# Optimization experiments

Measured on AMD Instinct MI355X. Metric: run time of the kernel, lower is better.

The kernel has to match this reference:

```python
import jax, jax.numpy as jnp
import numpy as np

FEATURE_MAPS = 128
POOLING_OUT = 4
KERNAL_LEN = 3
EMB_DIM = 300
CLASSES = 7
B, L, N = 64, 512, 2048


def setup_inputs() -> dict:
    key = jax.random.key(0)
    ks = jax.random.split(key, 10)
    sentence = jax.random.normal(ks[0], (B, 1, L, EMB_DIM), dtype=jnp.float32)
    # ROIs: [x1, x2) spans within [0, L], span length in [1, 32]
    x1 = jax.random.randint(ks[1], (N,), 0, L - 33)
    span = jax.random.randint(ks[2], (N,), 1, 33)
    rois = jnp.stack([x1, x1 + span], axis=1).astype(jnp.int64)
    ridx = jax.random.randint(ks[3], (N,), 0, B).astype(jnp.int64)
    s = 0.02
    conv_w = jax.random.normal(ks[4], (FEATURE_MAPS, 1, KERNAL_LEN, EMB_DIM), dtype=jnp.float32) * s
    conv_b = jax.random.normal(ks[5], (FEATURE_MAPS,), dtype=jnp.float32) * s
    FF = FEATURE_MAPS * POOLING_OUT
    fc1_w = jax.random.normal(ks[6], (FF, FF), dtype=jnp.float32) * s
    fc1_b = jax.random.normal(ks[7], (FF,), dtype=jnp.float32) * s
    cls_w = jax.random.normal(ks[8], (CLASSES + 1, FF), dtype=jnp.float32) * s
    cls_b = jax.random.normal(ks[9], (CLASSES + 1,), dtype=jnp.float32) * s
    return {"sentence": sentence, "rois": rois, "ridx": ridx,
            "conv_w": conv_w, "conv_b": conv_b, "fc1_w": fc1_w, "fc1_b": fc1_b,
            "cls_w": cls_w, "cls_b": cls_b}


def reference(sentence, rois, ridx, conv_w, conv_b, fc1_w, fc1_b, cls_w, cls_b):
    # conv1: Conv2d(1->F, (K, D), padding=(1,0)) + ReLU -> [B, F, L, 1]
    feat = jax.lax.conv_general_dilated(
        sentence, conv_w, window_strides=(1, 1),
        padding=((1, 1), (0, 0)),
        dimension_numbers=("NCHW", "OIHW", "NCHW"))
    feat = jax.nn.relu(feat + conv_b[None, :, None, None])[..., 0]  # [B, F, L]
    # ROI max-pool over each span [x1, x2) of the length dim (vectorized)
    g = feat[ridx]                                  # [N, F, L]
    pos = jnp.arange(feat.shape[-1])
    mask = (pos[None, :] >= rois[:, 0:1]) & (pos[None, :] < rois[:, 1:2])  # [N, L]
    neg = jnp.finfo(feat.dtype).min
    pooled = jnp.max(jnp.where(mask[:, None, :], g, neg), axis=-1)  # [N, F]
    # AdaptiveMaxPool2d((1, P)) with input width 1 replicates each channel P times,
    # and .view flattening is channel-major -> jnp.repeat along last axis matches.
    x = jnp.repeat(pooled, POOLING_OUT, axis=-1)    # [N, F*P]
    x = x @ fc1_w.T + fc1_b
    return x @ cls_w.T + cls_b                      # [N, CLASSES+1]
```

## Files before the change

### kernel.cpp

```cpp
#include <hip/hip_runtime.h>
#include <hip/hip_bf16.h>

#define FMAPS 128
#define SEQL  512
#define BATCH 64
#define EMB   300
#define NKC   30
#define NROI  2048
#define FFDIM 512
#define NCLS  8

#define MF_BLOCKS   32
#define B2_BLOCKS   1
#define WPAD_BLOCKS 480

typedef short bf16x8 __attribute__((ext_vector_type(8)));
typedef float f32x4  __attribute__((ext_vector_type(4)));

static __device__ __forceinline__ float relu_(float x) { return x > 0.f ? x : 0.f; }
static __device__ __forceinline__ uint bf16bits(float f) {
    __hip_bfloat16 h = __float2bfloat16(f);
    return (uint)*reinterpret_cast<ushort*>(&h);
}

__global__ __launch_bounds__(256) void prep(
    const float* __restrict__ conv_w, const float* __restrict__ cls_w,
    const float* __restrict__ fc1_w, const float* __restrict__ fc1_b,
    const float* __restrict__ cls_b,
    ushort* __restrict__ wf, float* __restrict__ Mfp, float* __restrict__ b2) {
    __shared__ float red[2][128];
    const int tid = threadIdx.x;
    int blk = blockIdx.x;

    if (blk < MF_BLOCKS) {
        const int c = blk & 7, q = blk >> 3;
        const int g = tid & 127, ih = tid >> 7;
        const int i0 = q * 128 + ih * 64;
        float s = 0.f;
        for (int i = i0; i < i0 + 64; ++i) {
            float4 w4 = *(const float4*)(fc1_w + (size_t)i * FFDIM + 4 * g);
            s = fmaf(cls_w[c * FFDIM + i], (w4.x + w4.y) + (w4.z + w4.w), s);
        }
        red[ih][g] = s;
        __syncthreads();
        if (tid < 128) Mfp[(q * 8 + c) * FMAPS + tid] = red[0][tid] + red[1][tid];
        return;
    }
    blk -= MF_BLOCKS;

    if (blk < B2_BLOCKS) {
        const int c = tid >> 5, l32 = tid & 31;
        float s = 0.f;
        for (int i = l32; i < FFDIM; i += 32)
            s = fmaf(cls_w[c * FFDIM + i], fc1_b[i], s);
#pragma unroll
        for (int off = 16; off; off >>= 1) s += __shfl_xor(s, off, 64);
        if (l32 == 0) b2[c] = s + cls_b[c];
        return;
    }
    blk -= B2_BLOCKS;

    {
        int idx = blk * 256 + tid;
        int j    = idx & 7;
        int lane = (idx >> 3) & 63;
        int nt   = (idx >> 9) & 7;
        int kc   = idx >> 12;
        int f = nt * 16 + (lane & 15);
        int k = kc * 32 + (lane >> 4) * 8 + j;
        int kr = k / 320, d = k % 320;
        float v = (d < EMB) ? conv_w[f * 900 + kr * 300 + d] : 0.f;
        wf[idx] = (ushort)bf16bits(v);
    }
}

__global__ __launch_bounds__(256) void conv_mfma(
    const float* __restrict__ sent, const ushort* __restrict__ wf,
    const float* __restrict__ cb, float* __restrict__ feat) {
    __shared__ __align__(16) ushort XL[66 * 320];
    const int t    = threadIdx.x;
    const int lane = t & 63;
    const int wn   = t >> 6;
    const int b    = blockIdx.x >> 3;
    const int l0   = (blockIdx.x & 7) << 6;
    const int mrow = lane & 15;
    const int koct = lane >> 4;

#pragma unroll
    for (int it = 0; it < 11; ++it) {
        int c = it * 256 + t;
        if (c < 2640) {
            int j = c / 40, i16 = c - j * 40;
            int sr = l0 + j - 1;
            int d0 = i16 * 8;
            float4 va = make_float4(0.f, 0.f, 0.f, 0.f), vb = va;
            if ((unsigned)sr < (unsigned)SEQL) {
                const float* srow = sent + ((size_t)b * SEQL + sr) * EMB;
                if (d0 < EMB)     va = *(const float4*)(srow + d0);
                if (d0 + 4 < EMB) vb = *(const float4*)(srow + d0 + 4);
            }
            uint4 pk;
            pk.x = bf16bits(va.x) | (bf16bits(va.y) << 16);
            pk.y = bf16bits(va.z) | (bf16bits(va.w) << 16);
            pk.z = bf16bits(vb.x) | (bf16bits(vb.y) << 16);
            pk.w = bf16bits(vb.z) | (bf16bits(vb.w) << 16);
            *(uint4*)((char*)XL + j * 640 + ((i16 ^ (j & 7)) << 4)) = pk;
        }
    }
    __syncthreads();

    f32x4 acc[4][2] = {};
    const ushort* wlane = wf + (size_t)(wn * 2) * 512 + (size_t)lane * 8;

#pragma unroll
    for (int kr = 0; kr < 3; ++kr) {
        const int sj = (mrow + kr) & 7;
#pragma unroll
        for (int dc = 0; dc < 10; ++dc) {
            const int kc = kr * 10 + dc;
            bf16x8 a[4];
#pragma unroll
            for (int mr = 0; mr < 4; ++mr) {
                const int j = mr * 16 + mrow + kr;
                a[mr] = *(const bf16x8*)((const char*)XL + j * 640 +
                                         (((dc * 4 + koct) ^ sj) << 4));
            }
            const ushort* wk = wlane + (size_t)kc * 4096;
            bf16x8 b0 = *(const bf16x8*)(wk);
            bf16x8 b1 = *(const bf16x8*)(wk + 512);
#pragma unroll
            for (int mr = 0; mr < 4; ++mr) {
                acc[mr][0] = __builtin_amdgcn_mfma_f32_16x16x32_bf16(a[mr], b0, acc[mr][0], 0, 0, 0);
                acc[mr][1] = __builtin_amdgcn_mfma_f32_16x16x32_bf16(a[mr], b1, acc[mr][1], 0, 0, 0);
            }
        }
    }

#pragma unroll
    for (int nr = 0; nr < 2; ++nr) {
        const int f = wn * 32 + nr * 16 + mrow;
        const float bias = cb[f];
#pragma unroll
        for (int mr = 0; mr < 4; ++mr) {
            const int lb = l0 + mr * 16 + koct * 4;
#pragma unroll
            for (int r = 0; r < 4; ++r)
                feat[((size_t)b * SEQL + (lb + r)) * FMAPS + f] = relu_(acc[mr][nr][r] + bias);
        }
    }
}

__global__ __launch_bounds__(256) void roi_fc(
    const float* __restrict__ feat, const int* __restrict__ rois,
    const int* __restrict__ ridx, const float* __restrict__ Mfp,
    const float* __restrict__ b2, float* __restrict__ out) {
    const int w    = threadIdx.x >> 6;
    const int lane = threadIdx.x & 63;
    const int n    = blockIdx.x * 4 + w;
    const int x1 = rois[n * 2 + 0];
    const int x2 = rois[n * 2 + 1];
    const int bi = ridx[n];
    const int half = lane >> 5, c4 = lane & 31;

    const float* base = feat + (size_t)bi * SEQL * FMAPS + c4 * 4;
    float4 m = make_float4(-1e30f, -1e30f, -1e30f, -1e30f);
    for (int l = x1 + half; l < x2; l += 2) {
        float4 v = *(const float4*)(base + (size_t)l * FMAPS);
        m.x = fmaxf(m.x, v.x); m.y = fmaxf(m.y, v.y);
        m.z = fmaxf(m.z, v.z); m.w = fmaxf(m.w, v.w);
    }
    m.x = fmaxf(m.x, __shfl_xor(m.x, 32, 64));
    m.y = fmaxf(m.y, __shfl_xor(m.y, 32, 64));
    m.z = fmaxf(m.z, __shfl_xor(m.z, 32, 64));
    m.w = fmaxf(m.w, __shfl_xor(m.w, 32, 64));

    const float4* M4 = (const float4*)Mfp;
#pragma unroll
    for (int c = 0; c < 8; ++c) {
        float4 w0 = M4[(c) * 32 + c4];
        float4 w1 = M4[(8 + c) * 32 + c4];
        float4 w2 = M4[(16 + c) * 32 + c4];
        float4 w3 = M4[(24 + c) * 32 + c4];
        float4 wv;
        wv.x = (w0.x + w1.x) + (w2.x + w3.x);
        wv.y = (w0.y + w1.y) + (w2.y + w3.y);
        wv.z = (w0.z + w1.z) + (w2.z + w3.z);
        wv.w = (w0.w + w1.w) + (w2.w + w3.w);
        float p = m.x * wv.x + m.y * wv.y + m.z * wv.z + m.w * wv.w;
#pragma unroll
        for (int off = 16; off; off >>= 1) p += __shfl_xor(p, off, 64);
        if (lane == 0) out[n * NCLS + c] = p + b2[c];
    }
}

extern "C" void kernel_launch(void* const* d_in, const int* in_sizes, int n_in,
                              void* d_out, int out_size, void* d_ws, size_t ws_size,
                              hipStream_t stream) {
    const float* sentence = (const float*)d_in[0];
    const int*   rois     = (const int*)d_in[1];
    const int*   ridx     = (const int*)d_in[2];
    const float* conv_w   = (const float*)d_in[3];
    const float* conv_b   = (const float*)d_in[4];
    const float* fc1_w    = (const float*)d_in[5];
    const float* fc1_b    = (const float*)d_in[6];
    const float* cls_w    = (const float*)d_in[7];
    const float* cls_b    = (const float*)d_in[8];
    float* out = (float*)d_out;

    char* ws = (char*)d_ws;
    float*  Ft  = (float*)ws;
    ushort* Wf  = (ushort*)(ws + 16777216);
    float*  Mfp = (float*)(ws + 16777216 + 245760);
    float*  b2  = Mfp + 4096;

    hipLaunchKernelGGL(prep, dim3(MF_BLOCKS + B2_BLOCKS + WPAD_BLOCKS), dim3(256), 0, stream,
                       conv_w, cls_w, fc1_w, fc1_b, cls_b, Wf, Mfp, b2);
    hipLaunchKernelGGL(conv_mfma, dim3((BATCH * SEQL) / 64), dim3(256), 0, stream,
                       sentence, Wf, conv_b, Ft);
    hipLaunchKernelGGL(roi_fc, dim3(NROI / 4), dim3(256), 0, stream,
                       Ft, rois, ridx, Mfp, b2, out);
}
```

Measured before the change: 132.2 us.

## Fuse prep, conv and ROI/FC kernels into one persistent kernel with grid barriers

Merges the three launches (weight prep, MFMA convolution, ROI pool plus FC) into a single 512-block kernel separated by software grid barriers built on atomics. The goal is to remove per-launch overhead and inter-kernel gaps. The Mfp partial-sum computation is now split across 64 blocks instead of 32, and the ROI stage sums 8 partials. The barrier assumes all 512 blocks are co-resident, which launch_bounds(256,2) is meant to ensure; if they are not, it risks deadlock. It also adds a memset and the spin-wait cost.

```diff
diff --git a/kernel.cpp b/kernel.cpp
--- a/kernel.cpp
+++ b/kernel.cpp
@@ -5,14 +5,10 @@
 #define SEQL  512
 #define BATCH 64
 #define EMB   300
-#define NKC   30
 #define NROI  2048
 #define FFDIM 512
 #define NCLS  8
-
-#define MF_BLOCKS   32
-#define B2_BLOCKS   1
-#define WPAD_BLOCKS 480
+#define GRID  512
 
 typedef short bf16x8 __attribute__((ext_vector_type(8)));
 typedef float f32x4  __attribute__((ext_vector_type(4)));
@@ -23,45 +19,39 @@
     return (uint)*reinterpret_cast<ushort*>(&h);
 }
 
-__global__ __launch_bounds__(256) void prep(
-    const float* __restrict__ conv_w, const float* __restrict__ cls_w,
+static __device__ __forceinline__ void grid_barrier(uint* bar, int tid) {
+    __syncthreads();
+    if (tid == 0) {
+        __threadfence();
+        uint g = __hip_atomic_load(bar + 1, __ATOMIC_RELAXED, __HIP_MEMORY_SCOPE_AGENT);
+        uint a = __hip_atomic_fetch_add(bar, 1u, __ATOMIC_ACQ_REL, __HIP_MEMORY_SCOPE_AGENT);
+        if (a == GRID - 1) {
+            __hip_atomic_store(bar, 0u, __ATOMIC_RELAXED, __HIP_MEMORY_SCOPE_AGENT);
+            __hip_atomic_store(bar + 1, g + 1u, __ATOMIC_RELEASE, __HIP_MEMORY_SCOPE_AGENT);
+        } else {
+            while (__hip_atomic_load(bar + 1, __ATOMIC_ACQUIRE, __HIP_MEMORY_SCOPE_AGENT) == g) {
+                __builtin_amdgcn_s_sleep(8);
+            }
+        }
+        __threadfence();
+    }
+    __syncthreads();
+}
+
+__global__ __launch_bounds__(256, 2) void rcnn_fused(
+    const float* __restrict__ sent, const int* __restrict__ rois,
+    const int* __restrict__ ridx, const float* __restrict__ conv_w,
+    const float* __restrict__ cb, const float* __restrict__ cls_w,
     const float* __restrict__ fc1_w, const float* __restrict__ fc1_b,
     const float* __restrict__ cls_b,
-    ushort* __restrict__ wf, float* __restrict__ Mfp, float* __restrict__ b2) {
-    __shared__ float red[2][128];
-    const int tid = threadIdx.x;
-    int blk = blockIdx.x;
-
-    if (blk < MF_BLOCKS) {
-        const int c = blk & 7, q = blk >> 3;
-        const int g = tid & 127, ih = tid >> 7;
-        const int i0 = q * 128 + ih * 64;
-        float s = 0.f;
-        for (int i = i0; i < i0 + 64; ++i) {
-            float4 w4 = *(const float4*)(fc1_w + (size_t)i * FFDIM + 4 * g);
-            s = fmaf(cls_w[c * FFDIM + i], (w4.x + w4.y) + (w4.z + w4.w), s);
-        }
-        red[ih][g] = s;
-        __syncthreads();
-        if (tid < 128) Mfp[(q * 8 + c) * FMAPS + tid] = red[0][tid] + red[1][tid];
-        return;
-    }
-    blk -= MF_BLOCKS;
-
-    if (blk < B2_BLOCKS) {
-        const int c = tid >> 5, l32 = tid & 31;
-        float s = 0.f;
-        for (int i = l32; i < FFDIM; i += 32)
-            s = fmaf(cls_w[c * FFDIM + i], fc1_b[i], s);
-#pragma unroll
-        for (int off = 16; off; off >>= 1) s += __shfl_xor(s, off, 64);
-        if (l32 == 0) b2[c] = s + cls_b[c];
-        return;
-    }
-    blk -= B2_BLOCKS;
-
-    {
-        int idx = blk * 256 + tid;
+    ushort* __restrict__ wf, float* __restrict__ Mfp, float* __restrict__ b2,
+    float* __restrict__ feat, float* __restrict__ out, uint* __restrict__ bar) {
+    __shared__ __align__(16) ushort XL[66 * 320];
+    const int t   = threadIdx.x;
+    const int blk = blockIdx.x;
+
+    if (t < 240) {
+        int idx  = blk * 240 + t;
         int j    = idx & 7;
         int lane = (idx >> 3) & 63;
         int nt   = (idx >> 9) & 7;
@@ -72,124 +62,138 @@
         float v = (d < EMB) ? conv_w[f * 900 + kr * 300 + d] : 0.f;
         wf[idx] = (ushort)bf16bits(v);
     }
-}
-
-__global__ __launch_bounds__(256) void conv_mfma(
-    const float* __restrict__ sent, const ushort* __restrict__ wf,
-    const float* __restrict__ cb, float* __restrict__ feat) {
-    __shared__ __align__(16) ushort XL[66 * 320];
-    const int t    = threadIdx.x;
-    const int lane = t & 63;
-    const int wn   = t >> 6;
-    const int b    = blockIdx.x >> 3;
-    const int l0   = (blockIdx.x & 7) << 6;
-    const int mrow = lane & 15;
-    const int koct = lane >> 4;
-
-#pragma unroll
-    for (int it = 0; it < 11; ++it) {
-        int c = it * 256 + t;
-        if (c < 2640) {
-            int j = c / 40, i16 = c - j * 40;
-            int sr = l0 + j - 1;
-            int d0 = i16 * 8;
-            float4 va = make_float4(0.f, 0.f, 0.f, 0.f), vb = va;
-            if ((unsigned)sr < (unsigned)SEQL) {
-                const float* srow = sent + ((size_t)b * SEQL + sr) * EMB;
-                if (d0 < EMB)     va = *(const float4*)(srow + d0);
-                if (d0 + 4 < EMB) vb = *(const float4*)(srow + d0 + 4);
-            }
-            uint4 pk;
-            pk.x = bf16bits(va.x) | (bf16bits(va.y) << 16);
-            pk.y = bf16bits(va.z) | (bf16bits(va.w) << 16);
-            pk.z = bf16bits(vb.x) | (bf16bits(vb.y) << 16);
-            pk.w = bf16bits(vb.z) | (bf16bits(vb.w) << 16);
-            *(uint4*)((char*)XL + j * 640 + ((i16 ^ (j & 7)) << 4)) = pk;
-        }
-    }
-    __syncthreads();
-
-    f32x4 acc[4][2] = {};
-    const ushort* wlane = wf + (size_t)(wn * 2) * 512 + (size_t)lane * 8;
-
-#pragma unroll
-    for (int kr = 0; kr < 3; ++kr) {
-        const int sj = (mrow + kr) & 7;
-#pragma unroll
-        for (int dc = 0; dc < 10; ++dc) {
-            const int kc = kr * 10 + dc;
-            bf16x8 a[4];
+    if (blk < 64) {
+        float* red = (float*)XL;
+        const int c = blk & 7, q8 = blk >> 3;
+        const int g = t & 127, ih = t >> 7;
+        const int i0 = q8 * 64 + ih * 32;
+        float s = 0.f;
+        for (int i = i0; i < i0 + 32; ++i) {
+            float4 w4 = *(const float4*)(fc1_w + (size_t)i * FFDIM + 4 * g);
+            s = fmaf(cls_w[c * FFDIM + i], (w4.x + w4.y) + (w4.z + w4.w), s);
+        }
+        red[ih * 128 + g] = s;
+        __syncthreads();
+        if (t < 128) Mfp[(q8 * 8 + c) * FMAPS + t] = red[t] + red[128 + t];
+    } else if (blk == 64) {
+        const int c = t >> 5, l32 = t & 31;
+        float s = 0.f;
+        for (int i = l32; i < FFDIM; i += 32)
+            s = fmaf(cls_w[c * FFDIM + i], fc1_b[i], s);
+#pragma unroll
+        for (int off = 16; off; off >>= 1) s += __shfl_xor(s, off, 64);
+        if (l32 == 0) b2[c] = s + cls_b[c];
+    }
+    grid_barrier(bar, t);
+
+    {
+        const int lane = t & 63;
+        const int wn   = t >> 6;
+        const int b    = blk >> 3;
+        const int l0   = (blk & 7) << 6;
+        const int mrow = lane & 15;
+        const int koct = lane >> 4;
+
+#pragma unroll
+        for (int it = 0; it < 11; ++it) {
+            int c = it * 256 + t;
+            if (c < 2640) {
+                int j = c / 40, i16 = c - j * 40;
+                int sr = l0 + j - 1;
+                int d0 = i16 * 8;
+                float4 va = make_float4(0.f, 0.f, 0.f, 0.f), vb = va;
+                if ((unsigned)sr < (unsigned)SEQL) {
+                    const float* srow = sent + ((size_t)b * SEQL + sr) * EMB;
+                    if (d0 < EMB)     va = *(const float4*)(srow + d0);
+                    if (d0 + 4 < EMB) vb = *(const float4*)(srow + d0 + 4);
+                }
+                uint4 pk;
+                pk.x = bf16bits(va.x) | (bf16bits(va.y) << 16);
+                pk.y = bf16bits(va.z) | (bf16bits(va.w) << 16);
+                pk.z = bf16bits(vb.x) | (bf16bits(vb.y) << 16);
+                pk.w = bf16bits(vb.z) | (bf16bits(vb.w) << 16);
+                *(uint4*)((char*)XL + j * 640 + ((i16 ^ (j & 7)) << 4)) = pk;
+            }
+        }
+        __syncthreads();
+
+        f32x4 acc[4][2] = {};
+        const ushort* wlane = wf + (size_t)(wn * 2) * 512 + (size_t)lane * 8;
+
+#pragma unroll
+        for (int kr = 0; kr < 3; ++kr) {
+            const int sj = (mrow + kr) & 7;
+#pragma unroll
+            for (int dc = 0; dc < 10; ++dc) {
+                const int kc = kr * 10 + dc;
+                bf16x8 a[4];
+#pragma unroll
+                for (int mr = 0; mr < 4; ++mr) {
+                    const int j = mr * 16 + mrow + kr;
+                    a[mr] = *(const bf16x8*)((const char*)XL + j * 640 +
+                                             (((dc * 4 + koct) ^ sj) << 4));
+                }
+                const ushort* wk = wlane + (size_t)kc * 4096;
+                bf16x8 b0 = *(const bf16x8*)(wk);
+                bf16x8 b1 = *(const bf16x8*)(wk + 512);
+#pragma unroll
+                for (int mr = 0; mr < 4; ++mr) {
+                    acc[mr][0] = __builtin_amdgcn_mfma_f32_16x16x32_bf16(a[mr], b0, acc[mr][0], 0, 0, 0);
+                    acc[mr][1] = __builtin_amdgcn_mfma_f32_16x16x32_bf16(a[mr], b1, acc[mr][1], 0, 0, 0);
+                }
+            }
+        }
+
+#pragma unroll
+        for (int nr = 0; nr < 2; ++nr) {
+            const int f = wn * 32 + nr * 16 + mrow;
+            const float bias = cb[f];
 #pragma unroll
             for (int mr = 0; mr < 4; ++mr) {
-                const int j = mr * 16 + mrow + kr;
-                a[mr] = *(const bf16x8*)((const char*)XL + j * 640 +
-                                         (((dc * 4 + koct) ^ sj) << 4));
-            }
-            const ushort* wk = wlane + (size_t)kc * 4096;
-            bf16x8 b0 = *(const bf16x8*)(wk);
-            bf16x8 b1 = *(const bf16x8*)(wk + 512);
-#pragma unroll
-            for (int mr = 0; mr < 4; ++mr) {
-                acc[mr][0] = __builtin_amdgcn_mfma_f32_16x16x32_bf16(a[mr], b0, acc[mr][0], 0, 0, 0);
-                acc[mr][1] = __builtin_amdgcn_mfma_f32_16x16x32_bf16(a[mr], b1, acc[mr][1], 0, 0, 0);
-            }
-        }
-    }
-
-#pragma unroll
-    for (int nr = 0; nr < 2; ++nr) {
-        const int f = wn * 32 + nr * 16 + mrow;
-        const float bias = cb[f];
-#pragma unroll
-        for (int mr = 0; mr < 4; ++mr) {
-            const int lb = l0 + mr * 16 + koct * 4;
-#pragma unroll
-            for (int r = 0; r < 4; ++r)
-                feat[((size_t)b * SEQL + (lb + r)) * FMAPS + f] = relu_(acc[mr][nr][r] + bias);
-        }
-    }
-}
-
-__global__ __launch_bounds__(256) void roi_fc(
-    const float* __restrict__ feat, const int* __restrict__ rois,
-    const int* __restrict__ ridx, const float* __restrict__ Mfp,
-    const float* __restrict__ b2, float* __restrict__ out) {
-    const int w    = threadIdx.x >> 6;
-    const int lane = threadIdx.x & 63;
-    const int n    = blockIdx.x * 4 + w;
-    const int x1 = rois[n * 2 + 0];
-    const int x2 = rois[n * 2 + 1];
-    const int bi = ridx[n];
-    const int half = lane >> 5, c4 = lane & 31;
-
-    const float* base = feat + (size_t)bi * SEQL * FMAPS + c4 * 4;
-    float4 m = make_float4(-1e30f, -1e30f, -1e30f, -1e30f);
-    for (int l = x1 + half; l < x2; l += 2) {
-        float4 v = *(const float4*)(base + (size_t)l * FMAPS);
-        m.x = fmaxf(m.x, v.x); m.y = fmaxf(m.y, v.y);
-        m.z = fmaxf(m.z, v.z); m.w = fmaxf(m.w, v.w);
-    }
-    m.x = fmaxf(m.x, __shfl_xor(m.x, 32, 64));
-    m.y = fmaxf(m.y, __shfl_xor(m.y, 32, 64));
-    m.z = fmaxf(m.z, __shfl_xor(m.z, 32, 64));
-    m.w = fmaxf(m.w, __shfl_xor(m.w, 32, 64));
-
-    const float4* M4 = (const float4*)Mfp;
-#pragma unroll
-    for (int c = 0; c < 8; ++c) {
-        float4 w0 = M4[(c) * 32 + c4];
-        float4 w1 = M4[(8 + c) * 32 + c4];
-        float4 w2 = M4[(16 + c) * 32 + c4];
-        float4 w3 = M4[(24 + c) * 32 + c4];
-        float4 wv;
-        wv.x = (w0.x + w1.x) + (w2.x + w3.x);
-        wv.y = (w0.y + w1.y) + (w2.y + w3.y);
-        wv.z = (w0.z + w1.z) + (w2.z + w3.z);
-        wv.w = (w0.w + w1.w) + (w2.w + w3.w);
-        float p = m.x * wv.x + m.y * wv.y + m.z * wv.z + m.w * wv.w;
-#pragma unroll
-        for (int off = 16; off; off >>= 1) p += __shfl_xor(p, off, 64);
-        if (lane == 0) out[n * NCLS + c] = p + b2[c];
+                const int lb = l0 + mr * 16 + koct * 4;
+#pragma unroll
+                for (int r = 0; r < 4; ++r)
+                    feat[((size_t)b * SEQL + (lb + r)) * FMAPS + f] = relu_(acc[mr][nr][r] + bias);
+            }
+        }
+    }
+    grid_barrier(bar, t);
+
+    {
+        const int w    = t >> 6;
+        const int lane = t & 63;
+        const int n    = blk * 4 + w;
+        const int x1 = rois[n * 2 + 0];
+        const int x2 = rois[n * 2 + 1];
+        const int bi = ridx[n];
+        const int half = lane >> 5, c4 = lane & 31;
+
+        const float* base = feat + (size_t)bi * SEQL * FMAPS + c4 * 4;
+        float4 m = make_float4(-1e30f, -1e30f, -1e30f, -1e30f);
+        for (int l = x1 + half; l < x2; l += 2) {
+            float4 v = *(const float4*)(base + (size_t)l * FMAPS);
+            m.x = fmaxf(m.x, v.x); m.y = fmaxf(m.y, v.y);
+            m.z = fmaxf(m.z, v.z); m.w = fmaxf(m.w, v.w);
+        }
+        m.x = fmaxf(m.x, __shfl_xor(m.x, 32, 64));
+        m.y = fmaxf(m.y, __shfl_xor(m.y, 32, 64));
+        m.z = fmaxf(m.z, __shfl_xor(m.z, 32, 64));
+        m.w = fmaxf(m.w, __shfl_xor(m.w, 32, 64));
+
+        const float4* M4 = (const float4*)Mfp;
+#pragma unroll
+        for (int c = 0; c < 8; ++c) {
+            float4 wv = make_float4(0.f, 0.f, 0.f, 0.f);
+#pragma unroll
+            for (int q = 0; q < 8; ++q) {
+                float4 wq = M4[(q * 8 + c) * 32 + c4];
+                wv.x += wq.x; wv.y += wq.y; wv.z += wq.z; wv.w += wq.w;
+            }
+            float p = m.x * wv.x + m.y * wv.y + m.z * wv.z + m.w * wv.w;
+#pragma unroll
+            for (int off = 16; off; off >>= 1) p += __shfl_xor(p, off, 64);
+            if (lane == 0) out[n * NCLS + c] = p + b2[c];
+        }
     }
 }
 
@@ -211,12 +215,11 @@
     float*  Ft  = (float*)ws;
     ushort* Wf  = (ushort*)(ws + 16777216);
     float*  Mfp = (float*)(ws + 16777216 + 245760);
-    float*  b2  = Mfp + 4096;
-
-    hipLaunchKernelGGL(prep, dim3(MF_BLOCKS + B2_BLOCKS + WPAD_BLOCKS), dim3(256), 0, stream,
-                       conv_w, cls_w, fc1_w, fc1_b, cls_b, Wf, Mfp, b2);
-    hipLaunchKernelGGL(conv_mfma, dim3((BATCH * SEQL) / 64), dim3(256), 0, stream,
-                       sentence, Wf, conv_b, Ft);
-    hipLaunchKernelGGL(roi_fc, dim3(NROI / 4), dim3(256), 0, stream,
-                       Ft, rois, ridx, Mfp, b2, out);
-}
+    float*  b2  = Mfp + 8192;
+    uint*   bar = (uint*)(ws + 16777216 + 245760 + 32768 + 256);
+
+    hipMemsetAsync(bar, 0, 16, stream);
+    hipLaunchKernelGGL(rcnn_fused, dim3(GRID), dim3(256), 0, stream,
+                       sentence, rois, ridx, conv_w, conv_b, cls_w,
+                       fc1_w, fc1_b, cls_b, Wf, Mfp, b2, Ft, out, bar);
+}
```

Result: slower. 315.7 us (+138.8%).

## Store conv features as bf16, halve conv tile rows, vectorize ROI pooling

Applied to the files above, without the earlier changes.

The conv output feature map is now written as bf16 instead of fp32, halving the intermediate buffer, and the ROI max-pool compares the raw bf16 bits as unsigned integers. That comparison is valid because post-ReLU values are non-negative. The conv kernel now uses 32-row tiles with twice as many blocks and a launch-bounds occupancy hint. ROI pooling is restructured so each lane loads 8 bf16 channels and covers 4 row groups with two loads per step, and the class dot product is spread across lane groups. This cuts write and read traffic for the intermediate but adds bf16 rounding of the features and duplicates more sentence halo rows per tile.

```diff
diff --git a/kernel.cpp b/kernel.cpp
--- a/kernel.cpp
+++ b/kernel.cpp
@@ -5,7 +5,6 @@
 #define SEQL  512
 #define BATCH 64
 #define EMB   300
-#define NKC   30
 #define NROI  2048
 #define FFDIM 512
 #define NCLS  8
@@ -14,13 +13,26 @@
 #define B2_BLOCKS   1
 #define WPAD_BLOCKS 480
 
-typedef short bf16x8 __attribute__((ext_vector_type(8)));
-typedef float f32x4  __attribute__((ext_vector_type(4)));
+typedef short  bf16x8 __attribute__((ext_vector_type(8)));
+typedef float  f32x4  __attribute__((ext_vector_type(4)));
+typedef ushort u16x8  __attribute__((ext_vector_type(8)));
 
 static __device__ __forceinline__ float relu_(float x) { return x > 0.f ? x : 0.f; }
 static __device__ __forceinline__ uint bf16bits(float f) {
     __hip_bfloat16 h = __float2bfloat16(f);
     return (uint)*reinterpret_cast<ushort*>(&h);
+}
+static __device__ __forceinline__ u16x8 umax8(u16x8 a, u16x8 b) {
+    u16x8 r;
+#pragma unroll
+    for (int j = 0; j < 8; ++j) r[j] = a[j] > b[j] ? a[j] : b[j];
+    return r;
+}
+static __device__ __forceinline__ u16x8 shfl8(u16x8 a, int off) {
+    union { u16x8 v; int i[4]; } s; s.v = a;
+#pragma unroll
+    for (int k = 0; k < 4; ++k) s.i[k] = __shfl_xor(s.i[k], off, 64);
+    return s.v;
 }
 
 __global__ __launch_bounds__(256) void prep(
@@ -74,22 +86,22 @@
     }
 }
 
-__global__ __launch_bounds__(256) void conv_mfma(
+__global__ __launch_bounds__(256, 4) void conv_mfma(
     const float* __restrict__ sent, const ushort* __restrict__ wf,
-    const float* __restrict__ cb, float* __restrict__ feat) {
-    __shared__ __align__(16) ushort XL[66 * 320];
+    const float* __restrict__ cb, ushort* __restrict__ feat) {
+    __shared__ __align__(16) ushort XL[34 * 320];
     const int t    = threadIdx.x;
     const int lane = t & 63;
     const int wn   = t >> 6;
-    const int b    = blockIdx.x >> 3;
-    const int l0   = (blockIdx.x & 7) << 6;
+    const int b    = blockIdx.x >> 4;
+    const int l0   = (blockIdx.x & 15) << 5;
     const int mrow = lane & 15;
     const int koct = lane >> 4;
 
 #pragma unroll
-    for (int it = 0; it < 11; ++it) {
+    for (int it = 0; it < 6; ++it) {
         int c = it * 256 + t;
-        if (c < 2640) {
+        if (c < 1360) {
             int j = c / 40, i16 = c - j * 40;
             int sr = l0 + j - 1;
             int d0 = i16 * 8;
@@ -109,7 +121,7 @@
     }
     __syncthreads();
 
-    f32x4 acc[4][2] = {};
+    f32x4 acc[2][2] = {};
     const ushort* wlane = wf + (size_t)(wn * 2) * 512 + (size_t)lane * 8;
 
 #pragma unroll
@@ -118,9 +130,9 @@
 #pragma unroll
         for (int dc = 0; dc < 10; ++dc) {
             const int kc = kr * 10 + dc;
-            bf16x8 a[4];
-#pragma unroll
-            for (int mr = 0; mr < 4; ++mr) {
+            bf16x8 a[2];
+#pragma unroll
+            for (int mr = 0; mr < 2; ++mr) {
                 const int j = mr * 16 + mrow + kr;
                 a[mr] = *(const bf16x8*)((const char*)XL + j * 640 +
                                          (((dc * 4 + koct) ^ sj) << 4));
@@ -129,7 +141,7 @@
             bf16x8 b0 = *(const bf16x8*)(wk);
             bf16x8 b1 = *(const bf16x8*)(wk + 512);
 #pragma unroll
-            for (int mr = 0; mr < 4; ++mr) {
+            for (int mr = 0; mr < 2; ++mr) {
                 acc[mr][0] = __builtin_amdgcn_mfma_f32_16x16x32_bf16(a[mr], b0, acc[mr][0], 0, 0, 0);
                 acc[mr][1] = __builtin_amdgcn_mfma_f32_16x16x32_bf16(a[mr], b1, acc[mr][1], 0, 0, 0);
             }
@@ -141,17 +153,18 @@
         const int f = wn * 32 + nr * 16 + mrow;
         const float bias = cb[f];
 #pragma unroll
-        for (int mr = 0; mr < 4; ++mr) {
+        for (int mr = 0; mr < 2; ++mr) {
             const int lb = l0 + mr * 16 + koct * 4;
 #pragma unroll
             for (int r = 0; r < 4; ++r)
-                feat[((size_t)b * SEQL + (lb + r)) * FMAPS + f] = relu_(acc[mr][nr][r] + bias);
+                feat[((size_t)b * SEQL + (lb + r)) * FMAPS + f] =
+                    (ushort)bf16bits(relu_(acc[mr][nr][r] + bias));
         }
     }
 }
 
 __global__ __launch_bounds__(256) void roi_fc(
-    const float* __restrict__ feat, const int* __restrict__ rois,
+    const ushort* __restrict__ feat, const int* __restrict__ rois,
     const int* __restrict__ ridx, const float* __restrict__ Mfp,
     const float* __restrict__ b2, float* __restrict__ out) {
     const int w    = threadIdx.x >> 6;
@@ -160,36 +173,40 @@
     const int x1 = rois[n * 2 + 0];
     const int x2 = rois[n * 2 + 1];
     const int bi = ridx[n];
-    const int half = lane >> 5, c4 = lane & 31;
-
-    const float* base = feat + (size_t)bi * SEQL * FMAPS + c4 * 4;
-    float4 m = make_float4(-1e30f, -1e30f, -1e30f, -1e30f);
-    for (int l = x1 + half; l < x2; l += 2) {
-        float4 v = *(const float4*)(base + (size_t)l * FMAPS);
-        m.x = fmaxf(m.x, v.x); m.y = fmaxf(m.y, v.y);
-        m.z = fmaxf(m.z, v.z); m.w = fmaxf(m.w, v.w);
-    }
-    m.x = fmaxf(m.x, __shfl_xor(m.x, 32, 64));
-    m.y = fmaxf(m.y, __shfl_xor(m.y, 32, 64));
-    m.z = fmaxf(m.z, __shfl_xor(m.z, 32, 64));
-    m.w = fmaxf(m.w, __shfl_xor(m.w, 32, 64));
-
-    const float4* M4 = (const float4*)Mfp;
-#pragma unroll
-    for (int c = 0; c < 8; ++c) {
-        float4 w0 = M4[(c) * 32 + c4];
-        float4 w1 = M4[(8 + c) * 32 + c4];
-        float4 w2 = M4[(16 + c) * 32 + c4];
-        float4 w3 = M4[(24 + c) * 32 + c4];
-        float4 wv;
-        wv.x = (w0.x + w1.x) + (w2.x + w3.x);
-        wv.y = (w0.y + w1.y) + (w2.y + w3.y);
-        wv.z = (w0.z + w1.z) + (w2.z + w3.z);
-        wv.w = (w0.w + w1.w) + (w2.w + w3.w);
-        float p = m.x * wv.x + m.y * wv.y + m.z * wv.z + m.w * wv.w;
-#pragma unroll
-        for (int off = 16; off; off >>= 1) p += __shfl_xor(p, off, 64);
-        if (lane == 0) out[n * NCLS + c] = p + b2[c];
+    const int c8 = lane & 15, rq = lane >> 4;
+
+    const ushort* base = feat + (size_t)bi * SEQL * FMAPS + c8 * 8;
+    u16x8 mx = (u16x8)0;
+    for (int l = x1 + rq; l < x2; l += 8) {
+        int l2 = min(l + 4, x2 - 1);
+        u16x8 v1 = *(const u16x8*)(base + (size_t)l  * FMAPS);
+        u16x8 v2 = *(const u16x8*)(base + (size_t)l2 * FMAPS);
+        mx = umax8(mx, umax8(v1, v2));
+    }
+    mx = umax8(mx, shfl8(mx, 16));
+    mx = umax8(mx, shfl8(mx, 32));
+
+    float pm[8];
+#pragma unroll
+    for (int j = 0; j < 8; ++j) pm[j] = __uint_as_float((uint)mx[j] << 16);
+
+#pragma unroll
+    for (int cc = 0; cc < 2; ++cc) {
+        const int c = rq * 2 + cc;
+        float4 wa = make_float4(0.f, 0.f, 0.f, 0.f), wb = wa;
+#pragma unroll
+        for (int q = 0; q < 4; ++q) {
+            const float* mrow = Mfp + (size_t)(q * 8 + c) * FMAPS + c8 * 8;
+            float4 aq = *(const float4*)mrow;
+            float4 bq = *(const float4*)(mrow + 4);
+            wa.x += aq.x; wa.y += aq.y; wa.z += aq.z; wa.w += aq.w;
+            wb.x += bq.x; wb.y += bq.y; wb.z += bq.z; wb.w += bq.w;
+        }
+        float p = pm[0] * wa.x + pm[1] * wa.y + pm[2] * wa.z + pm[3] * wa.w
+                + pm[4] * wb.x + pm[5] * wb.y + pm[6] * wb.z + pm[7] * wb.w;
+#pragma unroll
+        for (int off = 1; off <= 8; off <<= 1) p += __shfl_xor(p, off, 64);
+        if (c8 == 0) out[n * NCLS + c] = p + b2[c];
     }
 }
 
@@ -208,14 +225,14 @@
     float* out = (float*)d_out;
 
     char* ws = (char*)d_ws;
-    float*  Ft  = (float*)ws;
-    ushort* Wf  = (ushort*)(ws + 16777216);
-    float*  Mfp = (float*)(ws + 16777216 + 245760);
+    ushort* Ft  = (ushort*)ws;
+    ushort* Wf  = (ushort*)(ws + 8388608);
+    float*  Mfp = (float*)(ws + 8388608 + 245760);
     float*  b2  = Mfp + 4096;
 
     hipLaunchKernelGGL(prep, dim3(MF_BLOCKS + B2_BLOCKS + WPAD_BLOCKS), dim3(256), 0, stream,
                        conv_w, cls_w, fc1_w, fc1_b, cls_b, Wf, Mfp, b2);
-    hipLaunchKernelGGL(conv_mfma, dim3((BATCH * SEQL) / 64), dim3(256), 0, stream,
+    hipLaunchKernelGGL(conv_mfma, dim3(BATCH * (SEQL / 32)), dim3(256), 0, stream,
                        sentence, Wf, conv_b, Ft);
     hipLaunchKernelGGL(roi_fc, dim3(NROI / 4), dim3(256), 0, stream,
                        Ft, rois, ridx, Mfp, b2, out);
```

Measured after the change: 123.4 us. 6.7% less time.
